# Performance work log

Measured on AMD Instinct MI355X. Metric: run time of the kernel, lower is better.

Reference implementation:

```python
import jax, jax.numpy as jnp
import numpy as np
from jax import lax

B, T, N, D = 64, 128, 64, 64
Q, EMB, PLM = 5, 8, 768
ALPHA = 0.5  # rarity_alpha

def _mlp(x, W1, b1, W2, b2):
    return jax.nn.relu(x @ W1 + b1) @ W2 + b2

def setup_inputs() -> dict:
    key = jax.random.key(0)
    ks = jax.random.split(key, 16)
    def xav(k, shape):
        fan_in = shape[-2] if len(shape) > 1 else shape[0]
        return jax.random.normal(k, shape, jnp.float32) / np.sqrt(fan_in)
    obs_emb = jax.random.normal(ks[0], (B, T, N, D), jnp.float32)
    observed_mask = (jax.random.uniform(ks[1], (B, T, N)) < 0.5).astype(jnp.float32)
    lengths = jax.random.randint(ks[2], (B, 1), T // 2, T + 1).astype(jnp.int32)
    lengths = lengths.at[0, 0].set(T)  # ensure max(lengths) == T like torch loop bound
    avg_interval = jax.random.uniform(ks[3], (B, T, N), jnp.float32) * 10.0
    return {
        "obs_emb": obs_emb, "observed_mask": observed_mask,
        "lengths": lengths, "avg_interval": avg_interval,
        "var_plm_rep": jax.random.normal(ks[4], (N, PLM), jnp.float32),
        "rarity_W": jax.random.normal(ks[5], (N, N), jnp.float32),
        "Wf1": xav(ks[6], (PLM, 2 * D)), "bf1": jnp.zeros((2 * D,), jnp.float32),
        "Wf2": xav(ks[7], (2 * D, Q)), "bf2": jnp.zeros((Q,), jnp.float32),
        "Wg1": xav(ks[8], (PLM, 2 * D)), "bg1": jnp.zeros((2 * D,), jnp.float32),
        "Wg2": xav(ks[9], (2 * D, EMB)), "bg2": jnp.zeros((EMB,), jnp.float32),
        "Wu": xav(ks[10], (Q, 2 * D + 1, D)), "bu": xav(ks[11], (Q, D)),
        "Wr": xav(ks[12], (Q, 2 * D + 1, D)), "br": xav(ks[13], (Q, D)),
        "Wc": xav(ks[14], (Q, 2 * D + 1, D)), "bc": xav(ks[15], (Q, D)),
    }

def reference(obs_emb, observed_mask, lengths, avg_interval, var_plm_rep, rarity_W,
              Wf1, bf1, Wf2, bf2, Wg1, bg1, Wg2, bg2, Wu, bu, Wr, br, Wc, bc):
    Bb, Tt, Nn, Dd = obs_emb.shape
    m_all = observed_mask.astype(obs_emb.dtype)                 # [B,T,N]
    # plm reps are repeated across batch in torch -> batch-identical, keep [N,*]
    qv = _mlp(var_plm_rep, Wf1, bf1, Wf2, bf2)                  # [N,Q]
    ne = _mlp(var_plm_rep, Wg1, bg1, Wg2, bg2)                  # [N,EMB]
    ne = ne / jnp.linalg.norm(ne, axis=-1, keepdims=True)
    adj = jax.nn.softmax(ne @ ne.T, axis=-1)                    # [N,N]
    # time-invariant per-node hypernetwork weights (MLP_Param einsums hoisted)
    Wr_n = jnp.einsum('nq,qio->nio', qv, Wr); br_n = qv @ br    # [N,2D+1,D],[N,D]
    Wu_n = jnp.einsum('nq,qio->nio', qv, Wu); bu_n = qv @ bu
    Wc_n = jnp.einsum('nq,qio->nio', qv, Wc); bc_n = qv @ bc
    I = jnp.eye(Nn, dtype=obs_emb.dtype)
    var_total = m_all.sum(axis=1)                               # [B,N]
    lens = lengths[:, 0]

    def step(carry, inp):
        h, out = carry
        x_t, m_t, ai_t, t = inp                                 # [B,N,D],[B,N],[B,N],[]
        rs = ALPHA * jnp.tanh(ai_t / (var_total + 1.0))         # rarity score [B,N]
        x = jnp.concatenate([x_t, rs[..., None]], axis=-1)      # [B,N,D+1]
        combined = jnp.concatenate([x, h], axis=-1)             # [B,N,2D+1]
        R = -rarity_W[None] * jnp.abs(rs[:, :, None] - rs[:, None, :])
        am = m_t[:, :, None] * m_t[:, None, :]                  # masked adjacency support
        A = adj[None] * (1.0 + R) * am * (1.0 - I) + I          # [B,N,N]
        msg = jnp.einsum('bij,bjf->bif', A, combined)           # dense message passing
        r = jax.nn.sigmoid(jnp.einsum('bnf,nfo->bno', msg, Wr_n) + br_n)
        u = jax.nn.sigmoid(jnp.einsum('bnf,nfo->bno', msg, Wu_n) + bu_n)
        upd = m_t[..., None] > 0                                # observed-node scatter mask
        h_r = jnp.where(upd, r * h, h)
        comb2 = jnp.concatenate([x, h_r], axis=-1)              # NOTE: no adj matmul here (as in torch)
        cand = jnp.tanh(jnp.einsum('bnf,nfo->bno', comb2, Wc_n) + bc_n)
        h_new = jnp.where(upd, (1.0 - u) * h_r + u * cand, h)
        out_new = jnp.where((t == lens - 1)[:, None, None], h_new, out)
        return (h_new, out_new), None

    h0 = jnp.zeros((Bb, Nn, Dd), obs_emb.dtype)
    xs = (obs_emb.swapaxes(0, 1), m_all.swapaxes(0, 1),
          avg_interval.swapaxes(0, 1), jnp.arange(Tt))
    (_, out), _ = lax.scan(step, (h0, jnp.zeros_like(h0)), xs)
    return out
```

## Files before the change

### kernel.cpp

```cpp
#include <hip/hip_runtime.h>
#include <cstddef>
#include <cstdint>

#define B_ 64
#define T_ 128
#define N_ 64
#define D_ 64
#define Q_ 5
#define E_ 8
#define P_ 768
#define H_ 128

typedef _Float16 f16;
typedef _Float16 f16x2 __attribute__((ext_vector_type(2)));
typedef _Float16 f16x4 __attribute__((ext_vector_type(4)));
typedef _Float16 f16x8 __attribute__((ext_vector_type(8)));
typedef float f32x4 __attribute__((ext_vector_type(4)));

__device__ __forceinline__ float fast_sig(float x) {
  return 1.f / (1.f + __expf(-x));
}
__device__ __forceinline__ float fast_tanh(float x) {
  return 1.f - 2.f / (1.f + __expf(2.f * x));
}
__device__ __forceinline__ f16x8 splat8(f16 c) {
  return f16x8{c, c, c, c, c, c, c, c};
}

__global__ void k_mlps(const float* __restrict__ vpr,
                       const float* __restrict__ Wf1, const float* __restrict__ bf1,
                       const float* __restrict__ Wf2, const float* __restrict__ bf2,
                       const float* __restrict__ Wg1, const float* __restrict__ bg1,
                       const float* __restrict__ Wg2, const float* __restrict__ bg2,
                       float* __restrict__ qv, float* __restrict__ neb) {
  int n = blockIdx.x;
  int tid = threadIdx.x;
  __shared__ float v[P_];
  __shared__ float hf[H_];
  __shared__ float hg[H_];
  __shared__ float tmp[E_];

  for (int i = tid; i < P_; i += 256) v[i] = vpr[n * P_ + i];
  __syncthreads();

  if (tid < H_) {
    int j = tid;
    float a = bf1[j];
#pragma unroll 8
    for (int i = 0; i < P_; ++i) a += v[i] * Wf1[i * H_ + j];
    hf[j] = fmaxf(a, 0.f);
  } else {
    int j = tid - H_;
    float a = bg1[j];
#pragma unroll 8
    for (int i = 0; i < P_; ++i) a += v[i] * Wg1[i * H_ + j];
    hg[j] = fmaxf(a, 0.f);
  }
  __syncthreads();
  if (tid < Q_) {
    float a = bf2[tid];
    for (int j = 0; j < H_; ++j) a += hf[j] * Wf2[j * Q_ + tid];
    qv[n * Q_ + tid] = a;
  } else if (tid >= 8 && tid < 8 + E_) {
    int e = tid - 8;
    float a = bg2[e];
    for (int j = 0; j < H_; ++j) a += hg[j] * Wg2[j * E_ + e];
    tmp[e] = a;
  }
  __syncthreads();
  if (tid == 0) {
    float s = 0.f;
    for (int e = 0; e < E_; ++e) s += tmp[e] * tmp[e];
    float r = 1.f / sqrtf(s);
    for (int e = 0; e < E_; ++e) neb[n * E_ + e] = tmp[e] * r;
  }
}

__global__ void k_meta(const float* __restrict__ neb, const float* __restrict__ qv,
                       const float* __restrict__ br, const float* __restrict__ bu,
                       const float* __restrict__ bc,
                       const float* __restrict__ Wr, const float* __restrict__ Wu,
                       const float* __restrict__ Wc, const float* __restrict__ rarw,
                       f16x2* __restrict__ adjP, float* __restrict__ brn,
                       float* __restrict__ bun, float* __restrict__ bcn,
                       float* __restrict__ WrsR, float* __restrict__ WrsU,
                       float* __restrict__ WrsC) {
  int n = blockIdx.x;
  int j = threadIdx.x;
  float s = 0.f;
#pragma unroll
  for (int e = 0; e < E_; ++e) s += neb[n * E_ + e] * neb[j * E_ + e];
  float m = s;
  for (int off = 32; off; off >>= 1) m = fmaxf(m, __shfl_xor(m, off));
  float ex = __expf(s - m);
  float sum = ex;
  for (int off = 32; off; off >>= 1) sum += __shfl_xor(sum, off);
  float av = ex / sum;
  adjP[n * N_ + j] = f16x2{(f16)av, (f16)(av * rarw[n * N_ + j])};

  float pr = 0.f, pu = 0.f, pc = 0.f;
  float wr = 0.f, wu = 0.f, wc = 0.f;
#pragma unroll
  for (int q = 0; q < Q_; ++q) {
    float qq = qv[n * Q_ + q];
    pr += qq * br[q * D_ + j];
    pu += qq * bu[q * D_ + j];
    pc += qq * bc[q * D_ + j];
    wr += qq * Wr[((size_t)q * 129 + 64) * D_ + j];
    wu += qq * Wu[((size_t)q * 129 + 64) * D_ + j];
    wc += qq * Wc[((size_t)q * 129 + 64) * D_ + j];
  }
  brn[n * D_ + j] = pr;
  bun[n * D_ + j] = pu;
  bcn[n * D_ + j] = pc;
  WrsR[n * D_ + j] = wr;
  WrsU[n * D_ + j] = wu;
  WrsC[n * D_ + j] = wc;
}

__global__ void k_pack(const float* __restrict__ Wr, const float* __restrict__ Wu,
                       const float* __restrict__ Wc, f16* __restrict__ Wpk) {
  int bid = blockIdx.x;
  int nt = bid & 3;
  int kt = (bid >> 2) & 3;
  int q = (bid >> 4) % 5;
  int g = bid / 80;
  const float* W = (g == 0) ? Wr : ((g == 1) ? Wu : Wc);
  int l = threadIdx.x;
  int co = 16 * nt + (l & 15);
  f16* dst = Wpk + (size_t)bid * 512 + l * 8;
#pragma unroll
  for (int e = 0; e < 8; ++e) {
    int k = 32 * kt + 8 * (l >> 4) + e;
    int f = k + (k >= 64);
    dst[e] = (f16)W[((size_t)q * 129 + f) * D_ + co];
  }
}

__global__ void k_vt(const float* __restrict__ mask, float* __restrict__ vt) {
  int b = blockIdx.x;
  int n = threadIdx.x;
  float s = 0.f;
  for (int t = 0; t < T_; ++t) s += mask[(b * T_ + t) * N_ + n];
  vt[b * N_ + n] = s;
}

__global__ __launch_bounds__(256, 1) __attribute__((amdgpu_waves_per_eu(1, 1)))
void k_seq(const float* __restrict__ obs, const float* __restrict__ mask,
           const int* __restrict__ lengths, const float* __restrict__ ai,
           const f16x2* __restrict__ adjP,
           const float* __restrict__ brn, const float* __restrict__ bun,
           const float* __restrict__ bcn, const float* __restrict__ WrsR,
           const float* __restrict__ WrsU, const float* __restrict__ WrsC,
           const float* __restrict__ qv, const float* __restrict__ vt,
           const f16* __restrict__ Wpk, float* __restrict__ out) {
  __shared__ __align__(16) f16 combT[128 * 72];
  __shared__ __align__(16) f16 xA[64 * 72];
  __shared__ __align__(16) f16 actA[64 * 168];
  __shared__ __align__(16) f16 AP[64 * 88];
  __shared__ __align__(16) f16 qvS[64 * 8];
  __shared__ __align__(16) float rsS[N_];
  __shared__ __align__(16) float mS[N_];
  __shared__ __align__(16) float mrS[N_];

  const int tid = threadIdx.x;
  const int b = blockIdx.x;
  const int lane = tid & 63;
  const int wv = tid >> 6;
  const int lm = lane & 15;
  const int lq = lane >> 4;
  const int oc = 16 * wv + lm;

  const int pn = tid >> 2;
  const int pj = 16 * (tid & 3);

  f16x8 wW[3][4][5];
#pragma unroll
  for (int g = 0; g < 3; ++g)
#pragma unroll
    for (int kt = 0; kt < 4; ++kt)
#pragma unroll
      for (int q = 0; q < 5; ++q)
        wW[g][kt][q] = *(const f16x8*)(Wpk +
            ((size_t)(((g * 5 + q) * 4 + kt) * 4 + wv) * 64 + lane) * 8);

  f16x2 bR[8], bU[8], bC[8], wRs[8], wUs[8], wCs[8];
#pragma unroll
  for (int mt = 0; mt < 4; ++mt)
#pragma unroll
    for (int ii = 0; ii < 2; ++ii) {
      int n0 = 16 * mt + 4 * lq + 2 * ii;
      bR[2 * mt + ii]  = f16x2{(f16)brn[n0 * D_ + oc],  (f16)brn[(n0 + 1) * D_ + oc]};
      bU[2 * mt + ii]  = f16x2{(f16)bun[n0 * D_ + oc],  (f16)bun[(n0 + 1) * D_ + oc]};
      bC[2 * mt + ii]  = f16x2{(f16)bcn[n0 * D_ + oc],  (f16)bcn[(n0 + 1) * D_ + oc]};
      wRs[2 * mt + ii] = f16x2{(f16)WrsR[n0 * D_ + oc], (f16)WrsR[(n0 + 1) * D_ + oc]};
      wUs[2 * mt + ii] = f16x2{(f16)WrsU[n0 * D_ + oc], (f16)WrsU[(n0 + 1) * D_ + oc]};
      wCs[2 * mt + ii] = f16x2{(f16)WrsC[n0 * D_ + oc], (f16)WrsC[(n0 + 1) * D_ + oc]};
    }

  f16x2 adjR[16];
#pragma unroll
  for (int k = 0; k < 16; ++k) adjR[k] = adjP[pn * N_ + pj + k];

#pragma unroll
  for (int u2 = 0; u2 < 2; ++u2) {
    int idx = 2 * tid + u2;
    int n = idx >> 3, q = idx & 7;
    qvS[idx] = (q < Q_) ? (f16)qv[n * Q_ + q] : (f16)0.f;
  }
  for (int i = tid; i < 64 * 72; i += 256) combT[64 * 72 + i] = (f16)0.f;

  f32x4 h[4];
#pragma unroll
  for (int mt = 0; mt < 4; ++mt) h[mt] = f32x4{0.f, 0.f, 0.f, 0.f};

  const float* xb = obs + (size_t)b * T_ * (N_ * D_) + pn * D_ + pj;
  float4 xq0 = *(const float4*)(xb);
  float4 xq1 = *(const float4*)(xb + 4);
  float4 xq2 = *(const float4*)(xb + 8);
  float4 xq3 = *(const float4*)(xb + 12);
  float mCur = 0.f, aCur = 0.f, vtR = 0.f;
  if (tid < N_) {
    vtR = vt[b * N_ + tid];
    mCur = mask[(size_t)b * T_ * N_ + tid];
    aCur = ai[(size_t)b * T_ * N_ + tid];
  }
  const int lenm1 = lengths[b] - 1;
  __syncthreads();

  f16x8 qh[4];
#pragma unroll
  for (int mt = 0; mt < 4; ++mt) qh[mt] = *(const f16x8*)(qvS + (lm + 16 * mt) * 8);

  for (int t = 0; t < T_; ++t) {
    if (tid < N_) {
      mS[tid] = mCur;
      rsS[tid] = 0.5f * fast_tanh(aCur / (vtR + 1.f));
    }
    {
      f16x8 v0 = {(f16)xq0.x, (f16)xq0.y, (f16)xq0.z, (f16)xq0.w,
                  (f16)xq1.x, (f16)xq1.y, (f16)xq1.z, (f16)xq1.w};
      f16x8 v1 = {(f16)xq2.x, (f16)xq2.y, (f16)xq2.z, (f16)xq2.w,
                  (f16)xq3.x, (f16)xq3.y, (f16)xq3.z, (f16)xq3.w};
      *(f16x8*)(xA + pn * 72 + pj) = v0;
      *(f16x8*)(xA + pn * 72 + pj + 8) = v1;
    }
    __syncthreads();

    {
      float ri = rsS[pn], mi = mS[pn];
      f16x8 av0, av1;
#pragma unroll
      for (int k = 0; k < 16; ++k) {
        float a = ((float)adjR[k][0] -
                   (float)adjR[k][1] * fabsf(ri - rsS[pj + k])) * mi * mS[pj + k];
        if (pn == pj + k) a = 1.f;
        if (k < 8) av0[k] = (f16)a;
        else av1[k - 8] = (f16)a;
      }
      *(f16x8*)(AP + pn * 88 + pj) = av0;
      *(f16x8*)(AP + pn * 88 + pj + 8) = av1;

      int n0 = 16 * wv;
      f16x8 t0, t1;
#pragma unroll
      for (int k = 0; k < 8; ++k) t0[k] = xA[(n0 + k) * 72 + lane];
#pragma unroll
      for (int k = 0; k < 8; ++k) t1[k] = xA[(n0 + 8 + k) * 72 + lane];
      *(f16x8*)(combT + lane * 72 + n0) = t0;
      *(f16x8*)(combT + lane * 72 + n0 + 8) = t1;
    }
    __syncthreads();

    {
#pragma unroll
      for (int s = 0; s < 2; ++s) {
        int ft = 2 * wv + s;
#pragma unroll
        for (int mt = 0; mt < 4; ++mt) {
          f32x4 acc = {0.f, 0.f, 0.f, 0.f};
#pragma unroll
          for (int kt = 0; kt < 2; ++kt) {
            f16x8 aF = *(const f16x8*)(AP + (lm + 16 * mt) * 88 + 8 * lq + 32 * kt);
            f16x8 bF = *(const f16x8*)(combT + (lm + 16 * ft) * 72 + 8 * lq + 32 * kt);
            acc = __builtin_amdgcn_mfma_f32_16x16x32_f16(aF, bF, acc, 0, 0, 0);
          }
          int row = 16 * mt + 4 * lq;
          int col = 16 * ft + lm;
          actA[(row + 0) * 168 + col] = (f16)acc[0];
          actA[(row + 1) * 168 + col] = (f16)acc[1];
          actA[(row + 2) * 168 + col] = (f16)acc[2];
          actA[(row + 3) * 168 + col] = (f16)acc[3];
        }
      }
      f16x8 a0 = *(const f16x8*)(AP + pn * 88 + pj);
      f16x8 a1 = *(const f16x8*)(AP + pn * 88 + pj + 8);
      float s = 0.f;
#pragma unroll
      for (int k = 0; k < 8; ++k)
        s += (float)a0[k] * rsS[pj + k] + (float)a1[k] * rsS[pj + 8 + k];
      s += __shfl_xor(s, 1);
      s += __shfl_xor(s, 2);
      if ((tid & 3) == 0) mrS[pn] = s;
    }
    __syncthreads();

    f32x4 racc[4], uacc[4];
#pragma unroll
    for (int mt = 0; mt < 4; ++mt) {
      racc[mt] = f32x4{0.f, 0.f, 0.f, 0.f};
      uacc[mt] = f32x4{0.f, 0.f, 0.f, 0.f};
    }
#pragma unroll
    for (int kt = 0; kt < 4; ++kt) {
      f16x8 aF[4];
#pragma unroll
      for (int mt = 0; mt < 4; ++mt)
        aF[mt] = *(const f16x8*)(actA + (lm + 16 * mt) * 168 + 8 * lq + 32 * kt);
#pragma unroll
      for (int q = 0; q < 5; ++q) {
#pragma unroll
        for (int mt = 0; mt < 4; ++mt) {
          f16x8 as = aF[mt] * splat8(qh[mt][q]);
          racc[mt] = __builtin_amdgcn_mfma_f32_16x16x32_f16(as, wW[0][kt][q], racc[mt], 0, 0, 0);
          uacc[mt] = __builtin_amdgcn_mfma_f32_16x16x32_f16(as, wW[1][kt][q], uacc[mt], 0, 0, 0);
        }
      }
    }

    f16x2 upk[8], hrpk[8];
    {
#pragma unroll
      for (int mt = 0; mt < 4; ++mt) {
        float4 mr4 = *(const float4*)&mrS[16 * mt + 4 * lq];
        float4 m4 = *(const float4*)&mS[16 * mt + 4 * lq];
#pragma unroll
        for (int i = 0; i < 4; ++i) {
          int row = 16 * mt + 4 * lq + i;
          int ii = 2 * mt + (i >> 1);
          float pr = racc[mt][i] + (float)bR[ii][i & 1] + mr4[i] * (float)wRs[ii][i & 1];
          float pu = uacc[mt][i] + (float)bU[ii][i & 1] + mr4[i] * (float)wUs[ii][i & 1];
          float r = fast_sig(pr);
          float u = fast_sig(pu);
          float hr = (m4[i] > 0.f) ? r * h[mt][i] : h[mt][i];
          upk[ii][i & 1] = (f16)u;
          hrpk[ii][i & 1] = (f16)hr;
          AP[row * 88 + oc] = (f16)hr;
        }
      }
      if (t + 1 < T_) {
        const float* xn = xb + (size_t)(t + 1) * (N_ * D_);
        xq0 = *(const float4*)(xn);
        xq1 = *(const float4*)(xn + 4);
        xq2 = *(const float4*)(xn + 8);
        xq3 = *(const float4*)(xn + 12);
        if (tid < N_) {
          mCur = mask[((size_t)b * T_ + t + 1) * N_ + tid];
          aCur = ai[((size_t)b * T_ + t + 1) * N_ + tid];
        }
      }
    }
    __syncthreads();

    f32x4 cacc[4];
#pragma unroll
    for (int mt = 0; mt < 4; ++mt) cacc[mt] = f32x4{0.f, 0.f, 0.f, 0.f};
#pragma unroll
    for (int kt = 0; kt < 4; ++kt) {
      f16x8 aF[4];
#pragma unroll
      for (int mt = 0; mt < 4; ++mt) {
        if (kt < 2)
          aF[mt] = *(const f16x8*)(xA + (lm + 16 * mt) * 72 + 8 * lq + 32 * kt);
        else
          aF[mt] = *(const f16x8*)(AP + (lm + 16 * mt) * 88 + 8 * lq + 32 * (kt - 2));
      }
#pragma unroll
      for (int q = 0; q < 5; ++q) {
#pragma unroll
        for (int mt = 0; mt < 4; ++mt) {
          f16x8 as = aF[mt] * splat8(qh[mt][q]);
          cacc[mt] = __builtin_amdgcn_mfma_f32_16x16x32_f16(as, wW[2][kt][q], cacc[mt], 0, 0, 0);
        }
      }
    }

    {
#pragma unroll
      for (int mt = 0; mt < 4; ++mt) {
        float4 rs4 = *(const float4*)&rsS[16 * mt + 4 * lq];
        float4 m4 = *(const float4*)&mS[16 * mt + 4 * lq];
        f16x4 hq;
#pragma unroll
        for (int i = 0; i < 4; ++i) {
          int ii = 2 * mt + (i >> 1);
          float pc = cacc[mt][i] + (float)bC[ii][i & 1] + rs4[i] * (float)wCs[ii][i & 1];
          float cand = fast_tanh(pc);
          float u = (float)upk[ii][i & 1];
          float hr = (float)hrpk[ii][i & 1];
          float hn = (m4[i] > 0.f) ? (1.f - u) * hr + u * cand : h[mt][i];
          h[mt][i] = hn;
          hq[i] = (f16)hn;
        }
        *(f16x4*)(combT + (64 + oc) * 72 + 16 * mt + 4 * lq) = hq;
        if (t == lenm1) {
#pragma unroll
          for (int i = 0; i < 4; ++i)
            out[((size_t)b * N_ + 16 * mt + 4 * lq + i) * D_ + oc] = h[mt][i];
        }
      }
    }
    __syncthreads();
  }
}

extern "C" void kernel_launch(void* const* d_in, const int* in_sizes, int n_in,
                              void* d_out, int out_size, void* d_ws, size_t ws_size,
                              hipStream_t stream) {
  const float* obs  = (const float*)d_in[0];
  const float* mask = (const float*)d_in[1];
  const int*   lens = (const int*)d_in[2];
  const float* ai   = (const float*)d_in[3];
  const float* vpr  = (const float*)d_in[4];
  const float* rarw = (const float*)d_in[5];
  const float* Wf1 = (const float*)d_in[6],  *bf1 = (const float*)d_in[7];
  const float* Wf2 = (const float*)d_in[8],  *bf2 = (const float*)d_in[9];
  const float* Wg1 = (const float*)d_in[10], *bg1 = (const float*)d_in[11];
  const float* Wg2 = (const float*)d_in[12], *bg2 = (const float*)d_in[13];
  const float* Wu = (const float*)d_in[14], *bu = (const float*)d_in[15];
  const float* Wr = (const float*)d_in[16], *br = (const float*)d_in[17];
  const float* Wc = (const float*)d_in[18], *bc = (const float*)d_in[19];

  char* p = (char*)d_ws;
  auto carve = [&](size_t bytes) {
    char* r = p;
    p += (bytes + 255) & ~(size_t)255;
    return r;
  };
  float* qv   = (float*)carve(N_ * Q_ * 4);
  float* neb  = (float*)carve(N_ * E_ * 4);
  f16x2* adjP = (f16x2*)carve(N_ * N_ * 4);
  float* brn  = (float*)carve(N_ * D_ * 4);
  float* bun  = (float*)carve(N_ * D_ * 4);
  float* bcn  = (float*)carve(N_ * D_ * 4);
  float* WrsR = (float*)carve(N_ * D_ * 4);
  float* WrsU = (float*)carve(N_ * D_ * 4);
  float* WrsC = (float*)carve(N_ * D_ * 4);
  float* vt   = (float*)carve(B_ * N_ * 4);
  f16* Wpk    = (f16*)carve((size_t)3 * 5 * 4 * 4 * 64 * 8 * 2);

  k_mlps<<<N_, 256, 0, stream>>>(vpr, Wf1, bf1, Wf2, bf2, Wg1, bg1, Wg2, bg2, qv, neb);
  k_meta<<<N_, 64, 0, stream>>>(neb, qv, br, bu, bc, Wr, Wu, Wc, rarw,
                                adjP, brn, bun, bcn, WrsR, WrsU, WrsC);
  k_pack<<<240, 64, 0, stream>>>(Wr, Wu, Wc, Wpk);
  k_vt<<<B_, 64, 0, stream>>>(mask, vt);
  k_seq<<<B_, 256, 0, stream>>>(obs, mask, lens, ai, adjP,
                                brn, bun, bcn, WrsR, WrsU, WrsC,
                                qv, vt, Wpk, (float*)d_out);
}
```

Before: 2.146 ms.

## Process two batch elements per workgroup to interleave independent recurrences

Each workgroup now runs the sequential GRU recurrence for two batch elements, with duplicated shared buffers and register state, and the grid shrinks to half as many blocks. The intent is to give each wave two independent dependency chains per barrier, so MFMA and LDS latency can overlap and the per-step barrier cost is spread over two elements. The adjacency values move from per-thread registers to shared memory to free registers for the doubled state. The cost is half as many workgroups on a GPU with many CUs, which leaves most of the device idle, plus more register pressure under a one-wave-per-EU launch bound and more LDS use.

```diff
diff --git a/kernel.cpp b/kernel.cpp
--- a/kernel.cpp
+++ b/kernel.cpp
@@ -154,17 +154,18 @@
            const float* __restrict__ WrsU, const float* __restrict__ WrsC,
            const float* __restrict__ qv, const float* __restrict__ vt,
            const f16* __restrict__ Wpk, float* __restrict__ out) {
-  __shared__ __align__(16) f16 combT[128 * 72];
-  __shared__ __align__(16) f16 xA[64 * 72];
-  __shared__ __align__(16) f16 actA[64 * 168];
-  __shared__ __align__(16) f16 AP[64 * 88];
+  __shared__ __align__(16) f16 combT[2][128 * 72];
+  __shared__ __align__(16) f16 xA[2][64 * 72];
+  __shared__ __align__(16) f16 actA[2][64 * 168];
+  __shared__ __align__(16) f16 AP[2][64 * 88];
   __shared__ __align__(16) f16 qvS[64 * 8];
-  __shared__ __align__(16) float rsS[N_];
-  __shared__ __align__(16) float mS[N_];
-  __shared__ __align__(16) float mrS[N_];
+  __shared__ __align__(16) f16x2 adjS[64 * 64];
+  __shared__ __align__(16) float rsS[2][N_];
+  __shared__ __align__(16) float mS[2][N_];
+  __shared__ __align__(16) float mrS[2][N_];
 
   const int tid = threadIdx.x;
-  const int b = blockIdx.x;
+  const int b0 = 2 * blockIdx.x;
   const int lane = tid & 63;
   const int wv = tid >> 6;
   const int lm = lane & 15;
@@ -198,9 +199,7 @@
       wCs[2 * mt + ii] = f16x2{(f16)WrsC[n0 * D_ + oc], (f16)WrsC[(n0 + 1) * D_ + oc]};
     }
 
-  f16x2 adjR[16];
-#pragma unroll
-  for (int k = 0; k < 16; ++k) adjR[k] = adjP[pn * N_ + pj + k];
+  for (int i = tid; i < 64 * 64; i += 256) adjS[i] = adjP[i];
 
 #pragma unroll
   for (int u2 = 0; u2 < 2; ++u2) {
@@ -208,24 +207,35 @@
     int n = idx >> 3, q = idx & 7;
     qvS[idx] = (q < Q_) ? (f16)qv[n * Q_ + q] : (f16)0.f;
   }
-  for (int i = tid; i < 64 * 72; i += 256) combT[64 * 72 + i] = (f16)0.f;
-
-  f32x4 h[4];
-#pragma unroll
-  for (int mt = 0; mt < 4; ++mt) h[mt] = f32x4{0.f, 0.f, 0.f, 0.f};
-
-  const float* xb = obs + (size_t)b * T_ * (N_ * D_) + pn * D_ + pj;
-  float4 xq0 = *(const float4*)(xb);
-  float4 xq1 = *(const float4*)(xb + 4);
-  float4 xq2 = *(const float4*)(xb + 8);
-  float4 xq3 = *(const float4*)(xb + 12);
-  float mCur = 0.f, aCur = 0.f, vtR = 0.f;
-  if (tid < N_) {
-    vtR = vt[b * N_ + tid];
-    mCur = mask[(size_t)b * T_ * N_ + tid];
-    aCur = ai[(size_t)b * T_ * N_ + tid];
-  }
-  const int lenm1 = lengths[b] - 1;
+#pragma unroll
+  for (int bb = 0; bb < 2; ++bb)
+    for (int i = tid; i < 64 * 72; i += 256) combT[bb][64 * 72 + i] = (f16)0.f;
+
+  f32x4 h[2][4];
+#pragma unroll
+  for (int bb = 0; bb < 2; ++bb)
+#pragma unroll
+    for (int mt = 0; mt < 4; ++mt) h[bb][mt] = f32x4{0.f, 0.f, 0.f, 0.f};
+
+  const float* xb[2];
+  float4 xq0[2], xq1[2], xq2[2], xq3[2];
+  float mCur[2], aCur[2], vtR[2];
+  int lenm1[2];
+#pragma unroll
+  for (int bb = 0; bb < 2; ++bb) {
+    xb[bb] = obs + (size_t)(b0 + bb) * T_ * (N_ * D_) + pn * D_ + pj;
+    xq0[bb] = *(const float4*)(xb[bb]);
+    xq1[bb] = *(const float4*)(xb[bb] + 4);
+    xq2[bb] = *(const float4*)(xb[bb] + 8);
+    xq3[bb] = *(const float4*)(xb[bb] + 12);
+    mCur[bb] = 0.f; aCur[bb] = 0.f; vtR[bb] = 0.f;
+    if (tid < N_) {
+      vtR[bb] = vt[(b0 + bb) * N_ + tid];
+      mCur[bb] = mask[(size_t)(b0 + bb) * T_ * N_ + tid];
+      aCur[bb] = ai[(size_t)(b0 + bb) * T_ * N_ + tid];
+    }
+    lenm1[bb] = lengths[b0 + bb] - 1;
+  }
   __syncthreads();
 
   f16x8 qh[4];
@@ -233,46 +243,56 @@
   for (int mt = 0; mt < 4; ++mt) qh[mt] = *(const f16x8*)(qvS + (lm + 16 * mt) * 8);
 
   for (int t = 0; t < T_; ++t) {
-    if (tid < N_) {
-      mS[tid] = mCur;
-      rsS[tid] = 0.5f * fast_tanh(aCur / (vtR + 1.f));
-    }
+#pragma unroll
+    for (int bb = 0; bb < 2; ++bb) {
+      if (tid < N_) {
+        mS[bb][tid] = mCur[bb];
+        rsS[bb][tid] = 0.5f * fast_tanh(aCur[bb] / (vtR[bb] + 1.f));
+      }
+      f16x8 v0 = {(f16)xq0[bb].x, (f16)xq0[bb].y, (f16)xq0[bb].z, (f16)xq0[bb].w,
+                  (f16)xq1[bb].x, (f16)xq1[bb].y, (f16)xq1[bb].z, (f16)xq1[bb].w};
+      f16x8 v1 = {(f16)xq2[bb].x, (f16)xq2[bb].y, (f16)xq2[bb].z, (f16)xq2[bb].w,
+                  (f16)xq3[bb].x, (f16)xq3[bb].y, (f16)xq3[bb].z, (f16)xq3[bb].w};
+      *(f16x8*)(xA[bb] + pn * 72 + pj) = v0;
+      *(f16x8*)(xA[bb] + pn * 72 + pj + 8) = v1;
+    }
+    __syncthreads();
+
     {
-      f16x8 v0 = {(f16)xq0.x, (f16)xq0.y, (f16)xq0.z, (f16)xq0.w,
-                  (f16)xq1.x, (f16)xq1.y, (f16)xq1.z, (f16)xq1.w};
-      f16x8 v1 = {(f16)xq2.x, (f16)xq2.y, (f16)xq2.z, (f16)xq2.w,
-                  (f16)xq3.x, (f16)xq3.y, (f16)xq3.z, (f16)xq3.w};
-      *(f16x8*)(xA + pn * 72 + pj) = v0;
-      *(f16x8*)(xA + pn * 72 + pj + 8) = v1;
+      f16x2 adjL[16];
+      *(f16x8*)&adjL[0]  = *(const f16x8*)(adjS + pn * 64 + pj);
+      *(f16x8*)&adjL[4]  = *(const f16x8*)(adjS + pn * 64 + pj + 4);
+      *(f16x8*)&adjL[8]  = *(const f16x8*)(adjS + pn * 64 + pj + 8);
+      *(f16x8*)&adjL[12] = *(const f16x8*)(adjS + pn * 64 + pj + 12);
+#pragma unroll
+      for (int bb = 0; bb < 2; ++bb) {
+        float ri = rsS[bb][pn], mi = mS[bb][pn];
+        f16x8 av0, av1;
+#pragma unroll
+        for (int k = 0; k < 16; ++k) {
+          float a = ((float)adjL[k][0] -
+                     (float)adjL[k][1] * fabsf(ri - rsS[bb][pj + k])) * mi * mS[bb][pj + k];
+          if (pn == pj + k) a = 1.f;
+          if (k < 8) av0[k] = (f16)a;
+          else av1[k - 8] = (f16)a;
+        }
+        *(f16x8*)(AP[bb] + pn * 88 + pj) = av0;
+        *(f16x8*)(AP[bb] + pn * 88 + pj + 8) = av1;
+
+        int n0 = 16 * wv;
+        f16x8 t0, t1;
+#pragma unroll
+        for (int k = 0; k < 8; ++k) t0[k] = xA[bb][(n0 + k) * 72 + lane];
+#pragma unroll
+        for (int k = 0; k < 8; ++k) t1[k] = xA[bb][(n0 + 8 + k) * 72 + lane];
+        *(f16x8*)(combT[bb] + lane * 72 + n0) = t0;
+        *(f16x8*)(combT[bb] + lane * 72 + n0 + 8) = t1;
+      }
     }
     __syncthreads();
 
-    {
-      float ri = rsS[pn], mi = mS[pn];
-      f16x8 av0, av1;
-#pragma unroll
-      for (int k = 0; k < 16; ++k) {
-        float a = ((float)adjR[k][0] -
-                   (float)adjR[k][1] * fabsf(ri - rsS[pj + k])) * mi * mS[pj + k];
-        if (pn == pj + k) a = 1.f;
-        if (k < 8) av0[k] = (f16)a;
-        else av1[k - 8] = (f16)a;
-      }
-      *(f16x8*)(AP + pn * 88 + pj) = av0;
-      *(f16x8*)(AP + pn * 88 + pj + 8) = av1;
-
-      int n0 = 16 * wv;
-      f16x8 t0, t1;
-#pragma unroll
-      for (int k = 0; k < 8; ++k) t0[k] = xA[(n0 + k) * 72 + lane];
-#pragma unroll
-      for (int k = 0; k < 8; ++k) t1[k] = xA[(n0 + 8 + k) * 72 + lane];
-      *(f16x8*)(combT + lane * 72 + n0) = t0;
-      *(f16x8*)(combT + lane * 72 + n0 + 8) = t1;
-    }
-    __syncthreads();
-
-    {
+#pragma unroll
+    for (int bb = 0; bb < 2; ++bb) {
 #pragma unroll
       for (int s = 0; s < 2; ++s) {
         int ft = 2 * wv + s;
@@ -281,59 +301,59 @@
           f32x4 acc = {0.f, 0.f, 0.f, 0.f};
 #pragma unroll
           for (int kt = 0; kt < 2; ++kt) {
-            f16x8 aF = *(const f16x8*)(AP + (lm + 16 * mt) * 88 + 8 * lq + 32 * kt);
-            f16x8 bF = *(const f16x8*)(combT + (lm + 16 * ft) * 72 + 8 * lq + 32 * kt);
+            f16x8 aF = *(const f16x8*)(AP[bb] + (lm + 16 * mt) * 88 + 8 * lq + 32 * kt);
+            f16x8 bF = *(const f16x8*)(combT[bb] + (lm + 16 * ft) * 72 + 8 * lq + 32 * kt);
             acc = __builtin_amdgcn_mfma_f32_16x16x32_f16(aF, bF, acc, 0, 0, 0);
           }
           int row = 16 * mt + 4 * lq;
           int col = 16 * ft + lm;
-          actA[(row + 0) * 168 + col] = (f16)acc[0];
-          actA[(row + 1) * 168 + col] = (f16)acc[1];
-          actA[(row + 2) * 168 + col] = (f16)acc[2];
-          actA[(row + 3) * 168 + col] = (f16)acc[3];
-        }
-      }
-      f16x8 a0 = *(const f16x8*)(AP + pn * 88 + pj);
-      f16x8 a1 = *(const f16x8*)(AP + pn * 88 + pj + 8);
+          actA[bb][(row + 0) * 168 + col] = (f16)acc[0];
+          actA[bb][(row + 1) * 168 + col] = (f16)acc[1];
+          actA[bb][(row + 2) * 168 + col] = (f16)acc[2];
+          actA[bb][(row + 3) * 168 + col] = (f16)acc[3];
+        }
+      }
+      f16x8 a0 = *(const f16x8*)(AP[bb] + pn * 88 + pj);
+      f16x8 a1 = *(const f16x8*)(AP[bb] + pn * 88 + pj + 8);
       float s = 0.f;
 #pragma unroll
       for (int k = 0; k < 8; ++k)
-        s += (float)a0[k] * rsS[pj + k] + (float)a1[k] * rsS[pj + 8 + k];
+        s += (float)a0[k] * rsS[bb][pj + k] + (float)a1[k] * rsS[bb][pj + 8 + k];
       s += __shfl_xor(s, 1);
       s += __shfl_xor(s, 2);
-      if ((tid & 3) == 0) mrS[pn] = s;
+      if ((tid & 3) == 0) mrS[bb][pn] = s;
     }
     __syncthreads();
 
-    f32x4 racc[4], uacc[4];
-#pragma unroll
-    for (int mt = 0; mt < 4; ++mt) {
-      racc[mt] = f32x4{0.f, 0.f, 0.f, 0.f};
-      uacc[mt] = f32x4{0.f, 0.f, 0.f, 0.f};
-    }
-#pragma unroll
-    for (int kt = 0; kt < 4; ++kt) {
-      f16x8 aF[4];
-#pragma unroll
-      for (int mt = 0; mt < 4; ++mt)
-        aF[mt] = *(const f16x8*)(actA + (lm + 16 * mt) * 168 + 8 * lq + 32 * kt);
-#pragma unroll
-      for (int q = 0; q < 5; ++q) {
-#pragma unroll
-        for (int mt = 0; mt < 4; ++mt) {
-          f16x8 as = aF[mt] * splat8(qh[mt][q]);
-          racc[mt] = __builtin_amdgcn_mfma_f32_16x16x32_f16(as, wW[0][kt][q], racc[mt], 0, 0, 0);
-          uacc[mt] = __builtin_amdgcn_mfma_f32_16x16x32_f16(as, wW[1][kt][q], uacc[mt], 0, 0, 0);
-        }
-      }
-    }
-
-    f16x2 upk[8], hrpk[8];
-    {
+    f16x2 upk[2][8], hrpk[2][8];
+#pragma unroll
+    for (int bb = 0; bb < 2; ++bb) {
+      f32x4 racc[4], uacc[4];
 #pragma unroll
       for (int mt = 0; mt < 4; ++mt) {
-        float4 mr4 = *(const float4*)&mrS[16 * mt + 4 * lq];
-        float4 m4 = *(const float4*)&mS[16 * mt + 4 * lq];
+        racc[mt] = f32x4{0.f, 0.f, 0.f, 0.f};
+        uacc[mt] = f32x4{0.f, 0.f, 0.f, 0.f};
+      }
+#pragma unroll
+      for (int kt = 0; kt < 4; ++kt) {
+        f16x8 aF[4];
+#pragma unroll
+        for (int mt = 0; mt < 4; ++mt)
+          aF[mt] = *(const f16x8*)(actA[bb] + (lm + 16 * mt) * 168 + 8 * lq + 32 * kt);
+#pragma unroll
+        for (int q = 0; q < 5; ++q) {
+#pragma unroll
+          for (int mt = 0; mt < 4; ++mt) {
+            f16x8 as = aF[mt] * splat8(qh[mt][q]);
+            racc[mt] = __builtin_amdgcn_mfma_f32_16x16x32_f16(as, wW[0][kt][q], racc[mt], 0, 0, 0);
+            uacc[mt] = __builtin_amdgcn_mfma_f32_16x16x32_f16(as, wW[1][kt][q], uacc[mt], 0, 0, 0);
+          }
+        }
+      }
+#pragma unroll
+      for (int mt = 0; mt < 4; ++mt) {
+        float4 mr4 = *(const float4*)&mrS[bb][16 * mt + 4 * lq];
+        float4 m4 = *(const float4*)&mS[bb][16 * mt + 4 * lq];
 #pragma unroll
         for (int i = 0; i < 4; ++i) {
           int row = 16 * mt + 4 * lq + i;
@@ -342,71 +362,71 @@
           float pu = uacc[mt][i] + (float)bU[ii][i & 1] + mr4[i] * (float)wUs[ii][i & 1];
           float r = fast_sig(pr);
           float u = fast_sig(pu);
-          float hr = (m4[i] > 0.f) ? r * h[mt][i] : h[mt][i];
-          upk[ii][i & 1] = (f16)u;
-          hrpk[ii][i & 1] = (f16)hr;
-          AP[row * 88 + oc] = (f16)hr;
+          float hr = (m4[i] > 0.f) ? r * h[bb][mt][i] : h[bb][mt][i];
+          upk[bb][ii][i & 1] = (f16)u;
+          hrpk[bb][ii][i & 1] = (f16)hr;
+          AP[bb][row * 88 + oc] = (f16)hr;
         }
       }
       if (t + 1 < T_) {
-        const float* xn = xb + (size_t)(t + 1) * (N_ * D_);
-        xq0 = *(const float4*)(xn);
-        xq1 = *(const float4*)(xn + 4);
-        xq2 = *(const float4*)(xn + 8);
-        xq3 = *(const float4*)(xn + 12);
+        const float* xn = xb[bb] + (size_t)(t + 1) * (N_ * D_);
+        xq0[bb] = *(const float4*)(xn);
+        xq1[bb] = *(const float4*)(xn + 4);
+        xq2[bb] = *(const float4*)(xn + 8);
+        xq3[bb] = *(const float4*)(xn + 12);
         if (tid < N_) {
-          mCur = mask[((size_t)b * T_ + t + 1) * N_ + tid];
-          aCur = ai[((size_t)b * T_ + t + 1) * N_ + tid];
+          mCur[bb] = mask[((size_t)(b0 + bb) * T_ + t + 1) * N_ + tid];
+          aCur[bb] = ai[((size_t)(b0 + bb) * T_ + t + 1) * N_ + tid];
         }
       }
     }
     __syncthreads();
 
-    f32x4 cacc[4];
-#pragma unroll
-    for (int mt = 0; mt < 4; ++mt) cacc[mt] = f32x4{0.f, 0.f, 0.f, 0.f};
-#pragma unroll
-    for (int kt = 0; kt < 4; ++kt) {
-      f16x8 aF[4];
+#pragma unroll
+    for (int bb = 0; bb < 2; ++bb) {
+      f32x4 cacc[4];
+#pragma unroll
+      for (int mt = 0; mt < 4; ++mt) cacc[mt] = f32x4{0.f, 0.f, 0.f, 0.f};
+#pragma unroll
+      for (int kt = 0; kt < 4; ++kt) {
+        f16x8 aF[4];
+#pragma unroll
+        for (int mt = 0; mt < 4; ++mt) {
+          if (kt < 2)
+            aF[mt] = *(const f16x8*)(xA[bb] + (lm + 16 * mt) * 72 + 8 * lq + 32 * kt);
+          else
+            aF[mt] = *(const f16x8*)(AP[bb] + (lm + 16 * mt) * 88 + 8 * lq + 32 * (kt - 2));
+        }
+#pragma unroll
+        for (int q = 0; q < 5; ++q) {
+#pragma unroll
+          for (int mt = 0; mt < 4; ++mt) {
+            f16x8 as = aF[mt] * splat8(qh[mt][q]);
+            cacc[mt] = __builtin_amdgcn_mfma_f32_16x16x32_f16(as, wW[2][kt][q], cacc[mt], 0, 0, 0);
+          }
+        }
+      }
 #pragma unroll
       for (int mt = 0; mt < 4; ++mt) {
-        if (kt < 2)
-          aF[mt] = *(const f16x8*)(xA + (lm + 16 * mt) * 72 + 8 * lq + 32 * kt);
-        else
-          aF[mt] = *(const f16x8*)(AP + (lm + 16 * mt) * 88 + 8 * lq + 32 * (kt - 2));
-      }
-#pragma unroll
-      for (int q = 0; q < 5; ++q) {
-#pragma unroll
-        for (int mt = 0; mt < 4; ++mt) {
-          f16x8 as = aF[mt] * splat8(qh[mt][q]);
-          cacc[mt] = __builtin_amdgcn_mfma_f32_16x16x32_f16(as, wW[2][kt][q], cacc[mt], 0, 0, 0);
-        }
-      }
-    }
-
-    {
-#pragma unroll
-      for (int mt = 0; mt < 4; ++mt) {
-        float4 rs4 = *(const float4*)&rsS[16 * mt + 4 * lq];
-        float4 m4 = *(const float4*)&mS[16 * mt + 4 * lq];
+        float4 rs4 = *(const float4*)&rsS[bb][16 * mt + 4 * lq];
+        float4 m4 = *(const float4*)&mS[bb][16 * mt + 4 * lq];
         f16x4 hq;
 #pragma unroll
         for (int i = 0; i < 4; ++i) {
           int ii = 2 * mt + (i >> 1);
           float pc = cacc[mt][i] + (float)bC[ii][i & 1] + rs4[i] * (float)wCs[ii][i & 1];
           float cand = fast_tanh(pc);
-          float u = (float)upk[ii][i & 1];
-          float hr = (float)hrpk[ii][i & 1];
-          float hn = (m4[i] > 0.f) ? (1.f - u) * hr + u * cand : h[mt][i];
-          h[mt][i] = hn;
+          float u = (float)upk[bb][ii][i & 1];
+          float hr = (float)hrpk[bb][ii][i & 1];
+          float hn = (m4[i] > 0.f) ? (1.f - u) * hr + u * cand : h[bb][mt][i];
+          h[bb][mt][i] = hn;
           hq[i] = (f16)hn;
         }
-        *(f16x4*)(combT + (64 + oc) * 72 + 16 * mt + 4 * lq) = hq;
-        if (t == lenm1) {
+        *(f16x4*)(combT[bb] + (64 + oc) * 72 + 16 * mt + 4 * lq) = hq;
+        if (t == lenm1[bb]) {
 #pragma unroll
           for (int i = 0; i < 4; ++i)
-            out[((size_t)b * N_ + 16 * mt + 4 * lq + i) * D_ + oc] = h[mt][i];
+            out[((size_t)(b0 + bb) * N_ + 16 * mt + 4 * lq + i) * D_ + oc] = h[bb][mt][i];
         }
       }
     }
@@ -454,7 +474,7 @@
                                 adjP, brn, bun, bcn, WrsR, WrsU, WrsC);
   k_pack<<<240, 64, 0, stream>>>(Wr, Wu, Wc, Wpk);
   k_vt<<<B_, 64, 0, stream>>>(mask, vt);
-  k_seq<<<B_, 256, 0, stream>>>(obs, mask, lens, ai, adjP,
-                                brn, bun, bcn, WrsR, WrsU, WrsC,
-                                qv, vt, Wpk, (float*)d_out);
-}
+  k_seq<<<B_ / 2, 256, 0, stream>>>(obs, mask, lens, ai, adjP,
+                                    brn, bun, bcn, WrsR, WrsU, WrsC,
+                                    qv, vt, Wpk, (float*)d_out);
+}
```

Measured after the change: 4.499 ms. 2.1x slower.
